# Performance work log

Measured on AMD Instinct MI355X. Metric: run time of the kernel, lower is better.

Reference implementation:

```python
import jax, jax.numpy as jnp
import numpy as np

B, H, W = 64, 512, 512
HW = H * W
MIN_, MAX_ = 100, 100          # seeds sampled per image (bg, fg)
MIN_P, MAX_P = 0.3, 0.3        # candidate-pool fractions
FG_ERODE_K, FG_ERODE_ITER = 11, 1
KSZ = 3                        # dilation kernel for seed maps
IGNORE_IDX = -255
N_BG = int(MIN_P * H * W)      # static bottom-n pool size
EPS = 1e-8


def _minpool2d(x, k):  # morphological erosion of binary map (geodesic border)
    return jax.lax.reduce_window(x, np.inf, jax.lax.min, (k, k), (1, 1), 'SAME')


def _maxpool3d(x, k):  # morphological dilation over (b,h,w)
    return jax.lax.reduce_window(x, -np.inf, jax.lax.max, (1, k, k), (1, 1, 1), 'SAME')


def _gumbel(u):
    return -jnp.log(-jnp.log(u))


def _one_sample(cam, u_fg, u_bg, th):
    # cam: [H,W] in [0,1]; u_fg/u_bg: [HW] uniform(0,1); th: scalar threshold
    cam_q = jnp.floor(cam * 255.0)
    th = jnp.where(th == 0.0, 1.0, jnp.where(th == 255.0, 254.0, th))
    deg = cam.min() == cam.max()  # degenerate map -> no seeds
    roi = (cam_q > th).astype(jnp.float32)
    for _ in range(FG_ERODE_ITER):
        roi = _minpool2d(roi, FG_ERODE_K)

    # ---- foreground: top-n of cam*roi, weighted sample max_ w/o replacement
    camr = (cam * roi + EPS).reshape(HW)
    n_fg = jnp.floor(MAX_P * roi.sum()).astype(jnp.int32)
    order = jnp.argsort(-camr, stable=True)                 # descending stable
    rank = jnp.zeros(HW, jnp.int32).at[order].set(jnp.arange(HW, dtype=jnp.int32))
    mask = rank < n_fg
    logp = jnp.log(jnp.where(mask, camr, 1.0))              # weighted: p = cam value
    score = jnp.where(mask, logp + _gumbel(u_fg), -jnp.inf) # Gumbel top-k == multinomial w/o repl.
    _, sel = jax.lax.top_k(score, MAX_)
    valid = (jnp.arange(MAX_) < jnp.minimum(MAX_, n_fg)) & (n_fg > 0) & (~deg)
    fg = jnp.zeros(HW, jnp.int32).at[sel].set(valid.astype(jnp.int32))

    # ---- background: bottom-n of cam, weighted by relu(1-cam)+eps
    camb = (cam + EPS).reshape(HW)
    orderb = jnp.argsort(camb, stable=True)                 # ascending stable
    rankb = jnp.zeros(HW, jnp.int32).at[orderb].set(jnp.arange(HW, dtype=jnp.int32))
    maskb = rankb < N_BG
    pb = jax.nn.relu(1.0 - camb) + EPS
    scoreb = jnp.where(maskb, jnp.log(pb) + _gumbel(u_bg), -jnp.inf)
    _, selb = jax.lax.top_k(scoreb, MIN_)
    validb = (jnp.arange(MIN_) < min(MIN_, N_BG)) & (~deg)
    bg = jnp.zeros(HW, jnp.int32).at[selb].set(validb.astype(jnp.int32))

    return fg.reshape(H, W), bg.reshape(H, W)


def setup_inputs() -> dict:
    key = jax.random.key(0)
    k1, k2, k3, k4 = jax.random.split(key, 4)
    x = jax.random.uniform(k1, (B, 1, H, W), dtype=jnp.float32)
    roi_thresh = jax.random.randint(k2, (B,), 0, 200).astype(jnp.float32)
    u_fg = jax.random.uniform(k3, (B, HW), dtype=jnp.float32, minval=1e-6, maxval=1.0)
    u_bg = jax.random.uniform(k4, (B, HW), dtype=jnp.float32, minval=1e-6, maxval=1.0)
    return {"x": x, "roi_thresh": roi_thresh, "u_fg": u_fg, "u_bg": u_bg}


def reference(x, roi_thresh, u_fg, u_bg):
    cam = x[:, 0]  # [B,H,W]
    all_fg, all_bg = jax.vmap(_one_sample)(cam, u_fg, u_bg, roi_thresh)
    if KSZ > 1:
        all_fg = (_maxpool3d(all_fg.astype(jnp.float32), KSZ) > 0.5).astype(jnp.int32)
        all_bg = (_maxpool3d(all_bg.astype(jnp.float32), KSZ) > 0.5).astype(jnp.int32)
    outer = all_fg + all_bg
    all_fg = jnp.where(outer == 2, 0, all_fg)
    all_bg = jnp.where(outer == 2, 0, all_bg)
    out = jnp.full((B, H, W), IGNORE_IDX, dtype=jnp.int32)
    out = jnp.where(all_fg == 1, 1, out)
    out = jnp.where(all_bg == 1, 0, out)
    return out
```

## Files before the change

### kernel.cpp

```cpp
#include <hip/hip_runtime.h>

typedef unsigned int u32;

#define BB 64
#define HH 512
#define WW 512
#define HWP 262144
#define WPI 8192
#define NBV 8192
#define NBS 4096
#define EPSF 1e-8f
#define NBGK 78643
#define CAND_CAP 4096
#define SEL_CAP 128
#define PN 20


__device__ __forceinline__ int vbucket(float vb){
    int b = (int)(vb * 8192.0f);
    b = b < 0 ? 0 : b;
    return b > (NBV-1) ? (NBV-1) : b;
}
__device__ __forceinline__ int sbucket(float s){
    float a = (s + 24.0f) * (4096.0f / 44.0f);
    a = fmaxf(a, 0.0f);
    int b = (int)a;
    return b > (NBS-1) ? (NBS-1) : b;
}
__device__ __forceinline__ u32 flipf(float s){
    u32 u = __float_as_uint(s);
    u32 m = (u & 0x80000000u) ? 0xFFFFFFFFu : 0x80000000u;
    return u ^ m;
}


__global__ __launch_bounds__(256) void k_prep(const float* __restrict__ x,
        const float* __restrict__ thr, u32* __restrict__ roi0,
        u32* __restrict__ ghist_bg, u32* __restrict__ minb, u32* __restrict__ maxb,
        int* __restrict__ out)
{
    __shared__ u32 hist[NBV];
    __shared__ u32 words[256];
    for (int i = threadIdx.x; i < NBV; i += 256) hist[i] = 0u;
    words[threadIdx.x] = 0u;
    __syncthreads();
    int img = blockIdx.x >> 5;
    int blk = blockIdx.x & 31;
    int t = threadIdx.x;
    size_t base4 = (size_t)img * (HWP/4) + (size_t)blk * 2048;
    const float4* c4 = (const float4*)x + base4;
    int4* o4 = (int4*)out + base4;
    float th = thr[img];
    th = (th == 0.0f) ? 1.0f : ((th == 255.0f) ? 254.0f : th);
    u32 mn = 0xFFFFFFFFu, mx = 0u;
    #pragma unroll
    for (int k = 0; k < 8; k++){
        float4 v4 = c4[k*256 + t];
        float vv[4] = {v4.x, v4.y, v4.z, v4.w};
        u32 nib = 0u;
        #pragma unroll
        for (int c = 0; c < 4; c++){
            float v = vv[c];
            u32 ub = __float_as_uint(v);
            mn = mn < ub ? mn : ub;
            mx = mx > ub ? mx : ub;
            if (floorf(v * 255.0f) > th) nib |= (1u << c);
            atomicAdd(&hist[vbucket(v + EPSF)], 1u);
        }
        if (nib) atomicOr(&words[k*32 + (t>>3)], nib << ((t&7)*4));
        o4[k*256 + t] = make_int4(-255,-255,-255,-255);
    }
    for (int o = 32; o >= 1; o >>= 1){
        u32 m2 = __shfl_down(mn, o); mn = mn < m2 ? mn : m2;
        u32 m3 = __shfl_down(mx, o); mx = mx > m3 ? mx : m3;
    }
    if ((t & 63) == 0){
        atomicMin(&minb[img], mn);
        atomicMax(&maxb[img], mx);
    }
    __syncthreads();
    roi0[(size_t)img * WPI + blk*256 + t] = words[t];
    for (int i = t; i < NBV; i += 256){
        u32 h = hist[i];
        if (h) atomicAdd(&ghist_bg[(size_t)img*NBV + i], h);
    }
}

__global__ __launch_bounds__(256) void k_erode(const u32* __restrict__ roi0,
        u32* __restrict__ roiE, u32* __restrict__ roiSum)
{
    __shared__ u32 A[WPI];
    __shared__ u32 Bm[WPI];
    int img = blockIdx.x, t = threadIdx.x;
    const u32* src = roi0 + (size_t)img * WPI;
    for (int i = t; i < WPI; i += 256) A[i] = src[i];
    __syncthreads();
    for (int i = t; i < WPI; i += 256){
        int wr = i & 15;
        u32 cur = A[i];
        u32 left  = (wr > 0)  ? A[i-1] : 0xFFFFFFFFu;
        u32 right = (wr < 15) ? A[i+1] : 0xFFFFFFFFu;
        u32 res = cur;
        #pragma unroll
        for (int d = 1; d <= 5; d++){
            res &= (cur >> d) | (right << (32 - d));
            res &= (cur << d) | (left  >> (32 - d));
        }
        Bm[i] = res;
    }
    __syncthreads();
    if (t == 0) A[0] = 0u;
    __syncthreads();
    u32 cnt = 0u;
    u32* dst = roiE + (size_t)img * WPI;
    for (int i = t; i < WPI; i += 256){
        int r = i >> 4;
        u32 res = 0xFFFFFFFFu;
        #pragma unroll
        for (int d = -5; d <= 5; d++){
            int rr = r + d;
            if (rr >= 0 && rr < HH) res &= Bm[i + d*16];
        }
        dst[i] = res;
        cnt += __popc(res);
    }
    for (int o = 32; o >= 1; o >>= 1) cnt += __shfl_down(cnt, o);
    if ((t & 63) == 0) atomicAdd(&A[0], cnt);
    __syncthreads();
    if (t == 0) roiSum[img] = A[0];
}

__global__ __launch_bounds__(256) void k_fghist(const float* __restrict__ x, const u32* __restrict__ roiE,
        u32* __restrict__ ghist_fg)
{
    __shared__ u32 hist[NBV];
    __shared__ u32 words[256];
    for (int i = threadIdx.x; i < NBV; i += 256) hist[i] = 0u;
    int img = blockIdx.x >> 5;
    int blk = blockIdx.x & 31;
    int t = threadIdx.x;
    words[t] = roiE[(size_t)img*WPI + blk*256 + t];
    __syncthreads();
    const float4* c4 = (const float4*)x + (size_t)img * (HWP/4) + (size_t)blk * 2048;
    #pragma unroll
    for (int k = 0; k < 8; k++){
        u32 nib = (words[k*32 + (t>>3)] >> ((t&7)*4)) & 0xFu;
        if (nib){
            float4 v4 = c4[k*256 + t];
            float vv[4] = {v4.x, v4.y, v4.z, v4.w};
            #pragma unroll
            for (int c = 0; c < 4; c++){
                if ((nib >> c) & 1u) atomicAdd(&hist[vbucket(vv[c] + EPSF)], 1u);
            }
        }
    }
    __syncthreads();
    for (int i = t; i < NBV; i += 256){
        u32 h = hist[i];
        if (h) atomicAdd(&ghist_fg[(size_t)img*NBV + i], h);
    }
}

__global__ __launch_bounds__(256) void k_bound1(const u32* __restrict__ ghf, const u32* __restrict__ ghb,
        const u32* __restrict__ minb, const u32* __restrict__ maxb, const u32* __restrict__ roiSum,
        int* __restrict__ prm)
{
    int b = blockIdx.x, t = threadIdx.x;
    __shared__ int partial[256];
    __shared__ int res[2];
    int deg = (minb[b] == maxb[b]) ? 1 : 0;
    int nfg = (int)floorf(0.3f * (float)(int)roiSum[b]);
    int Bf = -1, rf = 0, Bb = -1, rb = 0;
    if (!deg && nfg > 0){
        const u32* hh = ghf + (size_t)b * NBV;
        int s = 0;
        for (int i = 0; i < 32; i++) s += (int)hh[NBV-1 - (t*32+i)];
        partial[t] = s;
        __syncthreads();
        if (t == 0){
            int cum = 0, q = 0;
            for (; q < 256; q++){ if (cum + partial[q] >= nfg) break; cum += partial[q]; }
            for (int i = 0; i < 32; i++){
                int bkt = NBV-1 - (q*32+i);
                int h = (int)hh[bkt];
                if (cum + h >= nfg){ res[0] = bkt; res[1] = nfg - cum; break; }
                cum += h;
            }
        }
        __syncthreads();
        Bf = res[0]; rf = res[1];
        __syncthreads();
    }
    if (!deg){
        const u32* hh = ghb + (size_t)b * NBV;
        int s = 0;
        for (int i = 0; i < 32; i++) s += (int)hh[t*32+i];
        partial[t] = s;
        __syncthreads();
        if (t == 0){
            int cum = 0, q = 0;
            for (; q < 256; q++){ if (cum + partial[q] >= NBGK) break; cum += partial[q]; }
            for (int i = 0; i < 32; i++){
                int bkt = q*32+i;
                int h = (int)hh[bkt];
                if (cum + h >= NBGK){ res[0] = bkt; res[1] = NBGK - cum; break; }
                cum += h;
            }
        }
        __syncthreads();
        Bb = res[0]; rb = res[1];
    }
    if (t == 0){
        int* p = prm + b * PN;
        p[0] = nfg; p[1] = deg; p[2] = Bf; p[3] = rf; p[4] = Bb; p[5] = rb;
    }
}

__global__ __launch_bounds__(256) void k_collect1(const float* __restrict__ x, const u32* __restrict__ roiE,
        const int* __restrict__ prm,
        uint2* __restrict__ candF, u32* __restrict__ cntF,
        uint2* __restrict__ candB, u32* __restrict__ cntB)
{
    __shared__ u32 words[256];
    int img = blockIdx.x >> 5;
    int blk = blockIdx.x & 31;
    int t = threadIdx.x;
    int Bf = prm[img*PN + 2];
    int Bb = prm[img*PN + 4];
    words[t] = roiE[(size_t)img*WPI + blk*256 + t];
    __syncthreads();
    const float4* c4 = (const float4*)x + (size_t)img * (HWP/4) + (size_t)blk * 2048;
    #pragma unroll
    for (int k = 0; k < 8; k++){
        float4 v4 = c4[k*256 + t];
        float vv[4] = {v4.x, v4.y, v4.z, v4.w};
        u32 nib = (words[k*32 + (t>>3)] >> ((t&7)*4)) & 0xFu;
        int pix0 = blk*8192 + k*1024 + t*4;
        #pragma unroll
        for (int c = 0; c < 4; c++){
            float vb = vv[c] + EPSF;
            int bkt = vbucket(vb);
            int pix = pix0 + c;
            if (bkt == Bb){
                u32 q = atomicAdd(&cntB[img], 1u);
                if (q < CAND_CAP) candB[(size_t)img*CAND_CAP + q] = make_uint2(__float_as_uint(vb), (u32)pix);
            }
            if (bkt == Bf && ((nib >> c) & 1u)){
                u32 q = atomicAdd(&cntF[img], 1u);
                if (q < CAND_CAP) candF[(size_t)img*CAND_CAP + q] = make_uint2(__float_as_uint(vb), (u32)pix);
            }
        }
    }
}

__global__ __launch_bounds__(256) void k_resolve1(const uint2* __restrict__ candF, const u32* __restrict__ cntF,
        const uint2* __restrict__ candB, const u32* __restrict__ cntB, int* __restrict__ prm)
{
    int b = blockIdx.x, t = threadIdx.x;
    __shared__ uint2 c[CAND_CAP];
    int rf = prm[b*PN + 3];
    if (rf > 0){
        int m = (int)cntF[b]; m = m < CAND_CAP ? m : CAND_CAP;
        for (int i = t; i < m; i += 256) c[i] = candF[(size_t)b*CAND_CAP + i];
        __syncthreads();
        for (int i = t; i < m; i += 256){
            u32 ki = c[i].x, xi = c[i].y;
            int r = 0;
            for (int j = 0; j < m; j++){
                u32 kj = c[j].x, xj = c[j].y;
                r += (kj > ki) || (kj == ki && xj < xi);
            }
            if (r == rf - 1){ prm[b*PN + 6] = (int)ki; prm[b*PN + 7] = (int)xi; }
        }
    } else if (t == 0){
        prm[b*PN + 6] = (int)0xFFFFFFFFu; prm[b*PN + 7] = -1;
    }
    __syncthreads();
    int rb = prm[b*PN + 5];
    if (rb > 0){
        int m = (int)cntB[b]; m = m < CAND_CAP ? m : CAND_CAP;
        for (int i = t; i < m; i += 256) c[i] = candB[(size_t)b*CAND_CAP + i];
        __syncthreads();
        for (int i = t; i < m; i += 256){
            u32 ki = c[i].x, xi = c[i].y;
            int r = 0;
            for (int j = 0; j < m; j++){
                u32 kj = c[j].x, xj = c[j].y;
                r += (kj < ki) || (kj == ki && xj < xi);
            }
            if (r == rb - 1){ prm[b*PN + 8] = (int)ki; prm[b*PN + 9] = (int)xi; }
        }
    } else if (t == 0){
        prm[b*PN + 8] = 0; prm[b*PN + 9] = -1;
    }
}

__global__ __launch_bounds__(256) void k_shist(const float* __restrict__ x, const u32* __restrict__ roiE,
        const float* __restrict__ ufg, const float* __restrict__ ubg, const int* __restrict__ prm,
        u32* __restrict__ shfG, u32* __restrict__ shbG)
{
    __shared__ u32 hf[NBS];
    __shared__ u32 hb[NBS];
    __shared__ u32 words[256];
    for (int i = threadIdx.x; i < NBS; i += 256){ hf[i] = 0u; hb[i] = 0u; }
    int img = blockIdx.x >> 5;
    int blk = blockIdx.x & 31;
    int t = threadIdx.x;
    words[t] = roiE[(size_t)img*WPI + blk*256 + t];
    __syncthreads();
    const int* p = prm + img*PN;
    u32 ubf = (u32)p[6]; int ibf = p[7];
    u32 ubb = (u32)p[8]; int ibb = p[9];
    size_t b4 = (size_t)img * (HWP/4) + (size_t)blk * 2048;
    const float4* c4 = (const float4*)x + b4;
    const float4* uf4 = (const float4*)ufg + b4;
    const float4* ub4 = (const float4*)ubg + b4;
    #pragma unroll
    for (int k = 0; k < 8; k++){
        float4 v4 = c4[k*256 + t];
        float vv[4] = {v4.x, v4.y, v4.z, v4.w};
        u32 nib = (words[k*32 + (t>>3)] >> ((t&7)*4)) & 0xFu;
        int pix0 = blk*8192 + k*1024 + t*4;
        float vbv[4]; bool fm[4], bm[4]; bool anyf = false, anyb = false;
        #pragma unroll
        for (int c = 0; c < 4; c++){
            float vb = vv[c] + EPSF;
            vbv[c] = vb;
            u32 bu = __float_as_uint(vb);
            int pix = pix0 + c;
            fm[c] = ((nib >> c) & 1u) && (bu > ubf || (bu == ubf && pix <= ibf));
            bm[c] = (bu < ubb || (bu == ubb && pix <= ibb));
            anyf |= fm[c]; anyb |= bm[c];
        }
        if (anyf){
            float4 u4 = uf4[k*256 + t];
            float uu[4] = {u4.x, u4.y, u4.z, u4.w};
            #pragma unroll
            for (int c = 0; c < 4; c++){
                if (fm[c]){
                    float s = logf(vbv[c]) - logf(-logf(uu[c]));
                    atomicAdd(&hf[sbucket(s)], 1u);
                }
            }
        }
        if (anyb){
            float4 u4 = ub4[k*256 + t];
            float uu[4] = {u4.x, u4.y, u4.z, u4.w};
            #pragma unroll
            for (int c = 0; c < 4; c++){
                if (bm[c]){
                    float pb = fmaxf(1.0f - vbv[c], 0.0f) + EPSF;
                    float s = logf(pb) - logf(-logf(uu[c]));
                    atomicAdd(&hb[sbucket(s)], 1u);
                }
            }
        }
    }
    __syncthreads();
    for (int i = t; i < NBS; i += 256){
        u32 h = hf[i]; if (h) atomicAdd(&shfG[(size_t)img*NBS + i], h);
        h = hb[i];     if (h) atomicAdd(&shbG[(size_t)img*NBS + i], h);
    }
}

__global__ __launch_bounds__(256) void k_bound2(const u32* __restrict__ shfG, const u32* __restrict__ shbG,
        int* __restrict__ prm)
{
    int b = blockIdx.x, t = threadIdx.x;
    __shared__ int partial[256];
    __shared__ int res[2];
    int* p = prm + b*PN;
    int nfg = p[0], deg = p[1];
    int kf = (deg || nfg <= 0) ? 0 : (nfg < 100 ? nfg : 100);
    int kb = deg ? 0 : 100;
    int sbf = 0x7FFFFFFF, needf = 0, sbb = 0x7FFFFFFF, needb = 0;
    if (kf > 0){
        const u32* hh = shfG + (size_t)b * NBS;
        int s = 0;
        for (int i = 0; i < 16; i++) s += (int)hh[NBS-1 - (t*16+i)];
        partial[t] = s;
        __syncthreads();
        if (t == 0){
            int cum = 0, q = 0;
            for (; q < 256; q++){ if (cum + partial[q] >= kf) break; cum += partial[q]; }
            for (int i = 0; i < 16; i++){
                int bkt = NBS-1 - (q*16+i);
                int h = (int)hh[bkt];
                if (cum + h >= kf){ res[0] = bkt; res[1] = kf - cum; break; }
                cum += h;
            }
        }
        __syncthreads();
        sbf = res[0]; needf = res[1];
        __syncthreads();
    }
    if (kb > 0){
        const u32* hh = shbG + (size_t)b * NBS;
        int s = 0;
        for (int i = 0; i < 16; i++) s += (int)hh[NBS-1 - (t*16+i)];
        partial[t] = s;
        __syncthreads();
        if (t == 0){
            int cum = 0, q = 0;
            for (; q < 256; q++){ if (cum + partial[q] >= kb) break; cum += partial[q]; }
            for (int i = 0; i < 16; i++){
                int bkt = NBS-1 - (q*16+i);
                int h = (int)hh[bkt];
                if (cum + h >= kb){ res[0] = bkt; res[1] = kb - cum; break; }
                cum += h;
            }
        }
        __syncthreads();
        sbb = res[0]; needb = res[1];
    }
    if (t == 0){
        p[10] = sbf; p[12] = needf; p[13] = sbb; p[15] = needb; p[16] = kf; p[17] = kb;
    }
}

__global__ __launch_bounds__(256) void k_collect2(const float* __restrict__ x, const u32* __restrict__ roiE,
        const float* __restrict__ ufg, const float* __restrict__ ubg, const int* __restrict__ prm,
        uint2* __restrict__ selF, u32* __restrict__ cntSelF, uint2* __restrict__ scandF, u32* __restrict__ cntScF,
        uint2* __restrict__ selB, u32* __restrict__ cntSelB, uint2* __restrict__ scandB, u32* __restrict__ cntScB)
{
    __shared__ u32 words[256];
    int img = blockIdx.x >> 5;
    int blk = blockIdx.x & 31;
    int t = threadIdx.x;
    words[t] = roiE[(size_t)img*WPI + blk*256 + t];
    __syncthreads();
    const int* p = prm + img*PN;
    u32 ubf = (u32)p[6]; int ibf = p[7];
    u32 ubb = (u32)p[8]; int ibb = p[9];
    int sbf = p[10], sbb = p[13];
    size_t b4 = (size_t)img * (HWP/4) + (size_t)blk * 2048;
    const float4* c4 = (const float4*)x + b4;
    const float4* uf4 = (const float4*)ufg + b4;
    const float4* ub4 = (const float4*)ubg + b4;
    #pragma unroll
    for (int k = 0; k < 8; k++){
        float4 v4 = c4[k*256 + t];
        float vv[4] = {v4.x, v4.y, v4.z, v4.w};
        u32 nib = (words[k*32 + (t>>3)] >> ((t&7)*4)) & 0xFu;
        int pix0 = blk*8192 + k*1024 + t*4;
        float vbv[4]; bool fm[4], bm[4]; bool anyf = false, anyb = false;
        #pragma unroll
        for (int c = 0; c < 4; c++){
            float vb = vv[c] + EPSF;
            vbv[c] = vb;
            u32 bu = __float_as_uint(vb);
            int pix = pix0 + c;
            fm[c] = ((nib >> c) & 1u) && (bu > ubf || (bu == ubf && pix <= ibf));
            bm[c] = (bu < ubb || (bu == ubb && pix <= ibb));
            anyf |= fm[c]; anyb |= bm[c];
        }
        if (anyf){
            float4 u4 = uf4[k*256 + t];
            float uu[4] = {u4.x, u4.y, u4.z, u4.w};
            #pragma unroll
            for (int c = 0; c < 4; c++){
                if (fm[c]){
                    float s = logf(vbv[c]) - logf(-logf(uu[c]));
                    int sb = sbucket(s);
                    if (sb > sbf){
                        u32 q = atomicAdd(&cntSelF[img], 1u);
                        if (q < SEL_CAP) selF[(size_t)img*SEL_CAP + q] = make_uint2(flipf(s), (u32)(pix0 + c));
                    } else if (sb == sbf){
                        u32 q = atomicAdd(&cntScF[img], 1u);
                        if (q < CAND_CAP) scandF[(size_t)img*CAND_CAP + q] = make_uint2(flipf(s), (u32)(pix0 + c));
                    }
                }
            }
        }
        if (anyb){
            float4 u4 = ub4[k*256 + t];
            float uu[4] = {u4.x, u4.y, u4.z, u4.w};
            #pragma unroll
            for (int c = 0; c < 4; c++){
                if (bm[c]){
                    float pb = fmaxf(1.0f - vbv[c], 0.0f) + EPSF;
                    float s = logf(pb) - logf(-logf(uu[c]));
                    int sb = sbucket(s);
                    if (sb > sbb){
                        u32 q = atomicAdd(&cntSelB[img], 1u);
                        if (q < SEL_CAP) selB[(size_t)img*SEL_CAP + q] = make_uint2(flipf(s), (u32)(pix0 + c));
                    } else if (sb == sbb){
                        u32 q = atomicAdd(&cntScB[img], 1u);
                        if (q < CAND_CAP) scandB[(size_t)img*CAND_CAP + q] = make_uint2(flipf(s), (u32)(pix0 + c));
                    }
                }
            }
        }
    }
}

__global__ __launch_bounds__(256) void k_final(
        const uint2* __restrict__ selF, const u32* __restrict__ cntSelF,
        const uint2* __restrict__ scandF, const u32* __restrict__ cntScF,
        const uint2* __restrict__ selB, const u32* __restrict__ cntSelB,
        const uint2* __restrict__ scandB, const u32* __restrict__ cntScB,
        const int* __restrict__ prm, int* __restrict__ out)
{
    int b = blockIdx.x, t = threadIdx.x;
    __shared__ uint2 c[CAND_CAP];
    __shared__ int seedF[SEL_CAP];
    __shared__ int seedB[SEL_CAP];
    __shared__ int nF, nB;
    const int* p = prm + b*PN;
    int needf = p[12], needb = p[15];

    int c0 = (int)cntSelF[b]; c0 = c0 < SEL_CAP ? c0 : SEL_CAP;
    for (int i = t; i < c0; i += 256) seedF[i] = (int)selF[(size_t)b*SEL_CAP + i].y;
    int m = (int)cntScF[b]; m = m < CAND_CAP ? m : CAND_CAP;
    for (int i = t; i < m; i += 256) c[i] = scandF[(size_t)b*CAND_CAP + i];
    if (t == 0){ nF = c0; nB = 0; }
    __syncthreads();
    for (int i = t; i < m; i += 256){
        u32 ki = c[i].x, xi = c[i].y;
        int r = 0;
        for (int j = 0; j < m; j++){
            u32 kj = c[j].x, xj = c[j].y;
            r += (kj > ki) || (kj == ki && xj < xi);
        }
        if (r < needf){
            int q = atomicAdd(&nF, 1);
            if (q < SEL_CAP) seedF[q] = (int)xi;
        }
    }
    __syncthreads();
    int fN = nF; fN = fN < SEL_CAP ? fN : SEL_CAP;
    __syncthreads();

    int c0b = (int)cntSelB[b]; c0b = c0b < SEL_CAP ? c0b : SEL_CAP;
    for (int i = t; i < c0b; i += 256) seedB[i] = (int)selB[(size_t)b*SEL_CAP + i].y;
    int mb = (int)cntScB[b]; mb = mb < CAND_CAP ? mb : CAND_CAP;
    for (int i = t; i < mb; i += 256) c[i] = scandB[(size_t)b*CAND_CAP + i];
    if (t == 0) nB = c0b;
    __syncthreads();
    for (int i = t; i < mb; i += 256){
        u32 ki = c[i].x, xi = c[i].y;
        int r = 0;
        for (int j = 0; j < mb; j++){
            u32 kj = c[j].x, xj = c[j].y;
            r += (kj > ki) || (kj == ki && xj < xi);
        }
        if (r < needb){
            int q = atomicAdd(&nB, 1);
            if (q < SEL_CAP) seedB[q] = (int)xi;
        }
    }
    __syncthreads();
    int bN = nB; bN = bN < SEL_CAP ? bN : SEL_CAP;
    __syncthreads();

    int* outp = out + (size_t)b * HWP;
    for (int task = t; task < fN * 9; task += 256){
        int s = seedF[task / 9];
        int o = task % 9;
        int y = (s >> 9) + (o / 3) - 1;
        int xx = (s & 511) + (o % 3) - 1;
        if (y < 0 || y >= HH || xx < 0 || xx >= WW) continue;
        bool conf = false;
        for (int j = 0; j < bN; j++){
            int sb2 = seedB[j];
            int dy = y - (sb2 >> 9); if (dy < 0) dy = -dy;
            int dx = xx - (sb2 & 511); if (dx < 0) dx = -dx;
            if (dy <= 1 && dx <= 1){ conf = true; break; }
        }
        if (!conf) outp[y * WW + xx] = 1;
    }
    for (int task = t; task < bN * 9; task += 256){
        int s = seedB[task / 9];
        int o = task % 9;
        int y = (s >> 9) + (o / 3) - 1;
        int xx = (s & 511) + (o % 3) - 1;
        if (y < 0 || y >= HH || xx < 0 || xx >= WW) continue;
        bool conf = false;
        for (int j = 0; j < fN; j++){
            int sf2 = seedF[j];
            int dy = y - (sf2 >> 9); if (dy < 0) dy = -dy;
            int dx = xx - (sf2 & 511); if (dx < 0) dx = -dx;
            if (dy <= 1 && dx <= 1){ conf = true; break; }
        }
        if (!conf) outp[y * WW + xx] = 0;
    }
}

extern "C" void kernel_launch(void* const* d_in, const int* in_sizes, int n_in,
                              void* d_out, int out_size, void* d_ws, size_t ws_size,
                              hipStream_t stream)
{
    (void)in_sizes; (void)n_in; (void)out_size; (void)ws_size;
    const float* x   = (const float*)d_in[0];
    const float* thr = (const float*)d_in[1];
    const float* ufg = (const float*)d_in[2];
    const float* ubg = (const float*)d_in[3];
    int* out = (int*)d_out;
    char* ws = (char*)d_ws;

    size_t off = 0;
    auto carve = [&](size_t bytes) -> char* {
        char* ptr = ws + off;
        off = (off + bytes + 255) & ~(size_t)255;
        return ptr;
    };
    u32* ghist_bg = (u32*)carve((size_t)BB*NBV*4);
    u32* ghist_fg = (u32*)carve((size_t)BB*NBV*4);
    u32* shf      = (u32*)carve((size_t)BB*NBS*4);
    u32* shb      = (u32*)carve((size_t)BB*NBS*4);
    u32* cnts     = (u32*)carve((size_t)6*BB*4);
    u32* maxb     = (u32*)carve((size_t)BB*4);
    u32* roiSum   = (u32*)carve((size_t)BB*4);
    size_t zero_bytes = off;
    u32* minb     = (u32*)carve((size_t)BB*4);
    size_t minb_off = (size_t)((char*)minb - ws);
    u32* roi0     = (u32*)carve((size_t)BB*WPI*4);
    u32* roiE     = (u32*)carve((size_t)BB*WPI*4);
    int* prm      = (int*)carve((size_t)BB*PN*4);
    uint2* candF  = (uint2*)carve((size_t)BB*CAND_CAP*8);
    uint2* candB  = (uint2*)carve((size_t)BB*CAND_CAP*8);
    uint2* scandF = (uint2*)carve((size_t)BB*CAND_CAP*8);
    uint2* scandB = (uint2*)carve((size_t)BB*CAND_CAP*8);
    uint2* selF   = (uint2*)carve((size_t)BB*SEL_CAP*8);
    uint2* selB   = (uint2*)carve((size_t)BB*SEL_CAP*8);
    u32* cntF = cnts, *cntB = cnts + BB, *cntSelF = cnts + 2*BB,
       *cntScF = cnts + 3*BB, *cntSelB = cnts + 4*BB, *cntScB = cnts + 5*BB;

    hipMemsetAsync(ws, 0, zero_bytes, stream);
    hipMemsetAsync(ws + minb_off, 0xFF, (size_t)BB*4, stream);

    k_prep    <<<2048, 256, 0, stream>>>(x, thr, roi0, ghist_bg, minb, maxb, out);
    k_erode   <<<64,   256, 0, stream>>>(roi0, roiE, roiSum);
    k_fghist  <<<2048, 256, 0, stream>>>(x, roiE, ghist_fg);
    k_bound1  <<<64,   256, 0, stream>>>(ghist_fg, ghist_bg, minb, maxb, roiSum, prm);
    k_collect1<<<2048, 256, 0, stream>>>(x, roiE, prm, candF, cntF, candB, cntB);
    k_resolve1<<<64,   256, 0, stream>>>(candF, cntF, candB, cntB, prm);
    k_shist   <<<2048, 256, 0, stream>>>(x, roiE, ufg, ubg, prm, shf, shb);
    k_bound2  <<<64,   256, 0, stream>>>(shf, shb, prm);
    k_collect2<<<2048, 256, 0, stream>>>(x, roiE, ufg, ubg, prm,
                                         selF, cntSelF, scandF, cntScF,
                                         selB, cntSelB, scandB, cntScB);
    k_final   <<<64,   256, 0, stream>>>(selF, cntSelF, scandF, cntScF,
                                         selB, cntSelB, scandB, cntScB, prm, out);
}
```

Measured before the change: 495.9 us.

## Fuse erosion into prep/fg-hist passes, shrink histograms, split final painting

```diff
diff --git a/kernel.cpp b/kernel.cpp
--- a/kernel.cpp
+++ b/kernel.cpp
@@ -7,8 +7,8 @@
 #define WW 512
 #define HWP 262144
 #define WPI 8192
-#define NBV 8192
-#define NBS 4096
+#define NBV 1024
+#define NBS 512
 #define EPSF 1e-8f
 #define NBGK 78643
 #define CAND_CAP 4096
@@ -17,12 +17,12 @@
 
 
 __device__ __forceinline__ int vbucket(float vb){
-    int b = (int)(vb * 8192.0f);
+    int b = (int)(vb * (float)NBV);
     b = b < 0 ? 0 : b;
     return b > (NBV-1) ? (NBV-1) : b;
 }
 __device__ __forceinline__ int sbucket(float s){
-    float a = (s + 24.0f) * (4096.0f / 44.0f);
+    float a = (s + 24.0f) * ((float)NBS / 44.0f);
     a = fmaxf(a, 0.0f);
     int b = (int)a;
     return b > (NBS-1) ? (NBS-1) : b;
@@ -33,23 +33,25 @@
     return u ^ m;
 }
 
+__device__ __forceinline__ void imgblk(int bid, int& img, int& blk){
+    int r = bid & 7, s = bid >> 3;
+    img = ((s >> 5) << 3) | r;
+    blk = s & 31;
+}
 
 __global__ __launch_bounds__(256) void k_prep(const float* __restrict__ x,
-        const float* __restrict__ thr, u32* __restrict__ roi0,
-        u32* __restrict__ ghist_bg, u32* __restrict__ minb, u32* __restrict__ maxb,
-        int* __restrict__ out)
+        const float* __restrict__ thr, u32* __restrict__ roiH,
+        u32* __restrict__ ghist_bg, u32* __restrict__ minb, u32* __restrict__ maxb)
 {
     __shared__ u32 hist[NBV];
-    __shared__ u32 words[256];
-    for (int i = threadIdx.x; i < NBV; i += 256) hist[i] = 0u;
-    words[threadIdx.x] = 0u;
-    __syncthreads();
-    int img = blockIdx.x >> 5;
-    int blk = blockIdx.x & 31;
+    __shared__ u32 A[256];
     int t = threadIdx.x;
-    size_t base4 = (size_t)img * (HWP/4) + (size_t)blk * 2048;
-    const float4* c4 = (const float4*)x + base4;
-    int4* o4 = (int4*)out + base4;
+    for (int i = t; i < NBV; i += 256) hist[i] = 0u;
+    A[t] = 0u;
+    __syncthreads();
+    int img, blk;
+    imgblk(blockIdx.x, img, blk);
+    const float4* c4 = (const float4*)x + (size_t)img * (HWP/4) + (size_t)blk * 2048;
     float th = thr[img];
     th = (th == 0.0f) ? 1.0f : ((th == 255.0f) ? 254.0f : th);
     u32 mn = 0xFFFFFFFFu, mx = 0u;
@@ -67,84 +69,62 @@
             if (floorf(v * 255.0f) > th) nib |= (1u << c);
             atomicAdd(&hist[vbucket(v + EPSF)], 1u);
         }
-        if (nib) atomicOr(&words[k*32 + (t>>3)], nib << ((t&7)*4));
-        o4[k*256 + t] = make_int4(-255,-255,-255,-255);
+        if (nib) atomicOr(&A[k*32 + (t>>3)], nib << ((t&7)*4));
     }
     for (int o = 32; o >= 1; o >>= 1){
         u32 m2 = __shfl_down(mn, o); mn = mn < m2 ? mn : m2;
         u32 m3 = __shfl_down(mx, o); mx = mx > m3 ? mx : m3;
     }
-    if ((t & 63) == 0){
-        atomicMin(&minb[img], mn);
-        atomicMax(&maxb[img], mx);
-    }
-    __syncthreads();
-    roi0[(size_t)img * WPI + blk*256 + t] = words[t];
-    for (int i = t; i < NBV; i += 256){
-        u32 h = hist[i];
-        if (h) atomicAdd(&ghist_bg[(size_t)img*NBV + i], h);
-    }
-}
-
-__global__ __launch_bounds__(256) void k_erode(const u32* __restrict__ roi0,
-        u32* __restrict__ roiE, u32* __restrict__ roiSum)
-{
-    __shared__ u32 A[WPI];
-    __shared__ u32 Bm[WPI];
-    int img = blockIdx.x, t = threadIdx.x;
-    const u32* src = roi0 + (size_t)img * WPI;
-    for (int i = t; i < WPI; i += 256) A[i] = src[i];
-    __syncthreads();
-    for (int i = t; i < WPI; i += 256){
-        int wr = i & 15;
-        u32 cur = A[i];
-        u32 left  = (wr > 0)  ? A[i-1] : 0xFFFFFFFFu;
-        u32 right = (wr < 15) ? A[i+1] : 0xFFFFFFFFu;
+    if ((t & 63) == 0){ atomicMin(&minb[img], mn); atomicMax(&maxb[img], mx); }
+    __syncthreads();
+    {
+        int wr = t & 15;
+        u32 cur = A[t];
+        u32 left  = (wr > 0)  ? A[t-1] : 0xFFFFFFFFu;
+        u32 right = (wr < 15) ? A[t+1] : 0xFFFFFFFFu;
         u32 res = cur;
         #pragma unroll
         for (int d = 1; d <= 5; d++){
             res &= (cur >> d) | (right << (32 - d));
             res &= (cur << d) | (left  >> (32 - d));
         }
-        Bm[i] = res;
-    }
-    __syncthreads();
-    if (t == 0) A[0] = 0u;
-    __syncthreads();
-    u32 cnt = 0u;
-    u32* dst = roiE + (size_t)img * WPI;
-    for (int i = t; i < WPI; i += 256){
-        int r = i >> 4;
-        u32 res = 0xFFFFFFFFu;
-        #pragma unroll
-        for (int d = -5; d <= 5; d++){
-            int rr = r + d;
-            if (rr >= 0 && rr < HH) res &= Bm[i + d*16];
-        }
-        dst[i] = res;
-        cnt += __popc(res);
-    }
+        roiH[(size_t)img*WPI + blk*256 + t] = res;
+    }
+    for (int i = t; i < NBV; i += 256){
+        u32 h = hist[i];
+        if (h) atomicAdd(&ghist_bg[(size_t)img*NBV + i], h);
+    }
+}
+
+__global__ __launch_bounds__(256) void k_vfg(const float* __restrict__ x,
+        const u32* __restrict__ roiH, u32* __restrict__ roiE,
+        u32* __restrict__ roiSum, u32* __restrict__ ghist_fg)
+{
+    __shared__ u32 hist[NBV];
+    __shared__ u32 W[256];
+    int t = threadIdx.x;
+    for (int i = t; i < NBV; i += 256) hist[i] = 0u;
+    int img, blk;
+    imgblk(blockIdx.x, img, blk);
+    const u32* rp = roiH + (size_t)img * WPI;
+    int iw = blk*256 + t;
+    int r = iw >> 4;
+    u32 res = 0xFFFFFFFFu;
+    #pragma unroll
+    for (int d = -5; d <= 5; d++){
+        int rr = r + d;
+        if (rr >= 0 && rr < HH) res &= rp[iw + d*16];
+    }
+    W[t] = res;
+    roiE[(size_t)img*WPI + iw] = res;
+    u32 cnt = __popc(res);
     for (int o = 32; o >= 1; o >>= 1) cnt += __shfl_down(cnt, o);
-    if ((t & 63) == 0) atomicAdd(&A[0], cnt);
-    __syncthreads();
-    if (t == 0) roiSum[img] = A[0];
-}
-
-__global__ __launch_bounds__(256) void k_fghist(const float* __restrict__ x, const u32* __restrict__ roiE,
-        u32* __restrict__ ghist_fg)
-{
-    __shared__ u32 hist[NBV];
-    __shared__ u32 words[256];
-    for (int i = threadIdx.x; i < NBV; i += 256) hist[i] = 0u;
-    int img = blockIdx.x >> 5;
-    int blk = blockIdx.x & 31;
-    int t = threadIdx.x;
-    words[t] = roiE[(size_t)img*WPI + blk*256 + t];
+    if ((t & 63) == 0) atomicAdd(&roiSum[img], cnt);
     __syncthreads();
     const float4* c4 = (const float4*)x + (size_t)img * (HWP/4) + (size_t)blk * 2048;
     #pragma unroll
     for (int k = 0; k < 8; k++){
-        u32 nib = (words[k*32 + (t>>3)] >> ((t&7)*4)) & 0xFu;
+        u32 nib = (W[k*32 + (t>>3)] >> ((t&7)*4)) & 0xFu;
         if (nib){
             float4 v4 = c4[k*256 + t];
             float vv[4] = {v4.x, v4.y, v4.z, v4.w};
@@ -174,14 +154,14 @@
     if (!deg && nfg > 0){
         const u32* hh = ghf + (size_t)b * NBV;
         int s = 0;
-        for (int i = 0; i < 32; i++) s += (int)hh[NBV-1 - (t*32+i)];
+        for (int i = 0; i < 4; i++) s += (int)hh[NBV-1 - (t*4+i)];
         partial[t] = s;
         __syncthreads();
         if (t == 0){
             int cum = 0, q = 0;
             for (; q < 256; q++){ if (cum + partial[q] >= nfg) break; cum += partial[q]; }
-            for (int i = 0; i < 32; i++){
-                int bkt = NBV-1 - (q*32+i);
+            for (int i = 0; i < 4; i++){
+                int bkt = NBV-1 - (q*4+i);
                 int h = (int)hh[bkt];
                 if (cum + h >= nfg){ res[0] = bkt; res[1] = nfg - cum; break; }
                 cum += h;
@@ -194,14 +174,14 @@
     if (!deg){
         const u32* hh = ghb + (size_t)b * NBV;
         int s = 0;
-        for (int i = 0; i < 32; i++) s += (int)hh[t*32+i];
+        for (int i = 0; i < 4; i++) s += (int)hh[t*4+i];
         partial[t] = s;
         __syncthreads();
         if (t == 0){
             int cum = 0, q = 0;
             for (; q < 256; q++){ if (cum + partial[q] >= NBGK) break; cum += partial[q]; }
-            for (int i = 0; i < 32; i++){
-                int bkt = q*32+i;
+            for (int i = 0; i < 4; i++){
+                int bkt = q*4+i;
                 int h = (int)hh[bkt];
                 if (cum + h >= NBGK){ res[0] = bkt; res[1] = NBGK - cum; break; }
                 cum += h;
@@ -222,8 +202,8 @@
         uint2* __restrict__ candB, u32* __restrict__ cntB)
 {
     __shared__ u32 words[256];
-    int img = blockIdx.x >> 5;
-    int blk = blockIdx.x & 31;
+    int img, blk;
+    imgblk(blockIdx.x, img, blk);
     int t = threadIdx.x;
     int Bf = prm[img*PN + 2];
     int Bb = prm[img*PN + 4];
@@ -302,10 +282,10 @@
     __shared__ u32 hf[NBS];
     __shared__ u32 hb[NBS];
     __shared__ u32 words[256];
-    for (int i = threadIdx.x; i < NBS; i += 256){ hf[i] = 0u; hb[i] = 0u; }
-    int img = blockIdx.x >> 5;
-    int blk = blockIdx.x & 31;
     int t = threadIdx.x;
+    for (int i = t; i < NBS; i += 256){ hf[i] = 0u; hb[i] = 0u; }
+    int img, blk;
+    imgblk(blockIdx.x, img, blk);
     words[t] = roiE[(size_t)img*WPI + blk*256 + t];
     __syncthreads();
     const int* p = prm + img*PN;
@@ -377,14 +357,14 @@
     if (kf > 0){
         const u32* hh = shfG + (size_t)b * NBS;
         int s = 0;
-        for (int i = 0; i < 16; i++) s += (int)hh[NBS-1 - (t*16+i)];
+        for (int i = 0; i < 2; i++) s += (int)hh[NBS-1 - (t*2+i)];
         partial[t] = s;
         __syncthreads();
         if (t == 0){
             int cum = 0, q = 0;
             for (; q < 256; q++){ if (cum + partial[q] >= kf) break; cum += partial[q]; }
-            for (int i = 0; i < 16; i++){
-                int bkt = NBS-1 - (q*16+i);
+            for (int i = 0; i < 2; i++){
+                int bkt = NBS-1 - (q*2+i);
                 int h = (int)hh[bkt];
                 if (cum + h >= kf){ res[0] = bkt; res[1] = kf - cum; break; }
                 cum += h;
@@ -397,14 +377,14 @@
     if (kb > 0){
         const u32* hh = shbG + (size_t)b * NBS;
         int s = 0;
-        for (int i = 0; i < 16; i++) s += (int)hh[NBS-1 - (t*16+i)];
+        for (int i = 0; i < 2; i++) s += (int)hh[NBS-1 - (t*2+i)];
         partial[t] = s;
         __syncthreads();
         if (t == 0){
             int cum = 0, q = 0;
             for (; q < 256; q++){ if (cum + partial[q] >= kb) break; cum += partial[q]; }
-            for (int i = 0; i < 16; i++){
-                int bkt = NBS-1 - (q*16+i);
+            for (int i = 0; i < 2; i++){
+                int bkt = NBS-1 - (q*2+i);
                 int h = (int)hh[bkt];
                 if (cum + h >= kb){ res[0] = bkt; res[1] = kb - cum; break; }
                 cum += h;
@@ -414,7 +394,7 @@
         sbb = res[0]; needb = res[1];
     }
     if (t == 0){
-        p[10] = sbf; p[12] = needf; p[13] = sbb; p[15] = needb; p[16] = kf; p[17] = kb;
+        p[10] = sbf; p[12] = needf; p[13] = sbb; p[15] = needb;
     }
 }
 
@@ -424,8 +404,8 @@
         uint2* __restrict__ selB, u32* __restrict__ cntSelB, uint2* __restrict__ scandB, u32* __restrict__ cntScB)
 {
     __shared__ u32 words[256];
-    int img = blockIdx.x >> 5;
-    int blk = blockIdx.x & 31;
+    int img, blk;
+    imgblk(blockIdx.x, img, blk);
     int t = threadIdx.x;
     words[t] = roiE[(size_t)img*WPI + blk*256 + t];
     __syncthreads();
@@ -494,12 +474,14 @@
     }
 }
 
-__global__ __launch_bounds__(256) void k_final(
+__global__ __launch_bounds__(256) void k_seeds(
         const uint2* __restrict__ selF, const u32* __restrict__ cntSelF,
         const uint2* __restrict__ scandF, const u32* __restrict__ cntScF,
         const uint2* __restrict__ selB, const u32* __restrict__ cntSelB,
         const uint2* __restrict__ scandB, const u32* __restrict__ cntScB,
-        const int* __restrict__ prm, int* __restrict__ out)
+        const int* __restrict__ prm,
+        int* __restrict__ gSeedF, int* __restrict__ gnF,
+        int* __restrict__ gSeedB, int* __restrict__ gnB)
 {
     int b = blockIdx.x, t = threadIdx.x;
     __shared__ uint2 c[CAND_CAP];
@@ -551,18 +533,37 @@
     }
     __syncthreads();
     int bN = nB; bN = bN < SEL_CAP ? bN : SEL_CAP;
-    __syncthreads();
-
-    int* outp = out + (size_t)b * HWP;
+
+    for (int i = t; i < fN; i += 256) gSeedF[b*SEL_CAP + i] = seedF[i];
+    for (int i = t; i < bN; i += 256) gSeedB[b*SEL_CAP + i] = seedB[i];
+    if (t == 0){ gnF[b] = fN; gnB[b] = bN; }
+}
+
+__global__ __launch_bounds__(256) void k_paint(
+        const int* __restrict__ gSeedF, const int* __restrict__ gnF,
+        const int* __restrict__ gSeedB, const int* __restrict__ gnB,
+        int* __restrict__ out)
+{
+    __shared__ int sF[SEL_CAP], sB[SEL_CAP];
+    int img = blockIdx.x >> 5, blk = blockIdx.x & 31, t = threadIdx.x;
+    int fN = gnF[img]; fN = fN < SEL_CAP ? fN : SEL_CAP;
+    int bN = gnB[img]; bN = bN < SEL_CAP ? bN : SEL_CAP;
+    for (int i = t; i < fN; i += 256) sF[i] = gSeedF[img*SEL_CAP + i];
+    for (int i = t; i < bN; i += 256) sB[i] = gSeedB[img*SEL_CAP + i];
+    int4* o4 = (int4*)(out + (size_t)img*HWP + blk*8192);
+    for (int i = t; i < 2048; i += 256) o4[i] = make_int4(-255,-255,-255,-255);
+    __syncthreads();
+    int row0 = blk * 16;
+    int* outp = out + (size_t)img*HWP;
     for (int task = t; task < fN * 9; task += 256){
-        int s = seedF[task / 9];
+        int s = sF[task / 9];
         int o = task % 9;
         int y = (s >> 9) + (o / 3) - 1;
         int xx = (s & 511) + (o % 3) - 1;
-        if (y < 0 || y >= HH || xx < 0 || xx >= WW) continue;
+        if (y < row0 || y >= row0 + 16 || xx < 0 || xx >= WW) continue;
         bool conf = false;
         for (int j = 0; j < bN; j++){
-            int sb2 = seedB[j];
+            int sb2 = sB[j];
             int dy = y - (sb2 >> 9); if (dy < 0) dy = -dy;
             int dx = xx - (sb2 & 511); if (dx < 0) dx = -dx;
             if (dy <= 1 && dx <= 1){ conf = true; break; }
@@ -570,14 +571,14 @@
         if (!conf) outp[y * WW + xx] = 1;
     }
     for (int task = t; task < bN * 9; task += 256){
-        int s = seedB[task / 9];
+        int s = sB[task / 9];
         int o = task % 9;
         int y = (s >> 9) + (o / 3) - 1;
         int xx = (s & 511) + (o % 3) - 1;
-        if (y < 0 || y >= HH || xx < 0 || xx >= WW) continue;
+        if (y < row0 || y >= row0 + 16 || xx < 0 || xx >= WW) continue;
         bool conf = false;
         for (int j = 0; j < fN; j++){
-            int sf2 = seedF[j];
+            int sf2 = sF[j];
             int dy = y - (sf2 >> 9); if (dy < 0) dy = -dy;
             int dx = xx - (sf2 & 511); if (dx < 0) dx = -dx;
             if (dy <= 1 && dx <= 1){ conf = true; break; }
@@ -609,12 +610,12 @@
     u32* shf      = (u32*)carve((size_t)BB*NBS*4);
     u32* shb      = (u32*)carve((size_t)BB*NBS*4);
     u32* cnts     = (u32*)carve((size_t)6*BB*4);
+    u32* roiSum   = (u32*)carve((size_t)BB*4);
     u32* maxb     = (u32*)carve((size_t)BB*4);
-    u32* roiSum   = (u32*)carve((size_t)BB*4);
     size_t zero_bytes = off;
     u32* minb     = (u32*)carve((size_t)BB*4);
     size_t minb_off = (size_t)((char*)minb - ws);
-    u32* roi0     = (u32*)carve((size_t)BB*WPI*4);
+    u32* roiH     = (u32*)carve((size_t)BB*WPI*4);
     u32* roiE     = (u32*)carve((size_t)BB*WPI*4);
     int* prm      = (int*)carve((size_t)BB*PN*4);
     uint2* candF  = (uint2*)carve((size_t)BB*CAND_CAP*8);
@@ -623,15 +624,18 @@
     uint2* scandB = (uint2*)carve((size_t)BB*CAND_CAP*8);
     uint2* selF   = (uint2*)carve((size_t)BB*SEL_CAP*8);
     uint2* selB   = (uint2*)carve((size_t)BB*SEL_CAP*8);
+    int* gSeedF   = (int*)carve((size_t)BB*SEL_CAP*4);
+    int* gSeedB   = (int*)carve((size_t)BB*SEL_CAP*4);
+    int* gnF      = (int*)carve((size_t)BB*4);
+    int* gnB      = (int*)carve((size_t)BB*4);
     u32* cntF = cnts, *cntB = cnts + BB, *cntSelF = cnts + 2*BB,
        *cntScF = cnts + 3*BB, *cntSelB = cnts + 4*BB, *cntScB = cnts + 5*BB;
 
     hipMemsetAsync(ws, 0, zero_bytes, stream);
     hipMemsetAsync(ws + minb_off, 0xFF, (size_t)BB*4, stream);
 
-    k_prep    <<<2048, 256, 0, stream>>>(x, thr, roi0, ghist_bg, minb, maxb, out);
-    k_erode   <<<64,   256, 0, stream>>>(roi0, roiE, roiSum);
-    k_fghist  <<<2048, 256, 0, stream>>>(x, roiE, ghist_fg);
+    k_prep    <<<2048, 256, 0, stream>>>(x, thr, roiH, ghist_bg, minb, maxb);
+    k_vfg     <<<2048, 256, 0, stream>>>(x, roiH, roiE, roiSum, ghist_fg);
     k_bound1  <<<64,   256, 0, stream>>>(ghist_fg, ghist_bg, minb, maxb, roiSum, prm);
     k_collect1<<<2048, 256, 0, stream>>>(x, roiE, prm, candF, cntF, candB, cntB);
     k_resolve1<<<64,   256, 0, stream>>>(candF, cntF, candB, cntB, prm);
@@ -640,6 +644,8 @@
     k_collect2<<<2048, 256, 0, stream>>>(x, roiE, ufg, ubg, prm,
                                          selF, cntSelF, scandF, cntScF,
                                          selB, cntSelB, scandB, cntScB);
-    k_final   <<<64,   256, 0, stream>>>(selF, cntSelF, scandF, cntScF,
-                                         selB, cntSelB, scandB, cntScB, prm, out);
-}
+    k_seeds   <<<64,   256, 0, stream>>>(selF, cntSelF, scandF, cntScF,
+                                         selB, cntSelB, scandB, cntScB, prm,
+                                         gSeedF, gnF, gSeedB, gnB);
+    k_paint   <<<2048, 256, 0, stream>>>(gSeedF, gnF, gSeedB, gnB, out);
+}
```

Measured after the change: 517.0 us. 4.2% more time.
